# Optimization experiments

Measured on AMD Instinct MI355X. Metric: run time of the kernel, lower is better.

Reference implementation:

```python
import jax, jax.numpy as jnp
import numpy as np

N, D, H_ENC, NZ, K, H_EXP, C = 32768, 1024, 512, 64, 16, 256, 10


def setup_inputs() -> dict:
    key = jax.random.key(0)
    ks = jax.random.split(key, 12)
    s = 0.02
    return {
        "X": jax.random.normal(ks[0], (N, D), dtype=jnp.float32),
        "enc_W": jax.random.normal(ks[1], (D, H_ENC), dtype=jnp.float32) * s,
        "enc_b": jnp.zeros((H_ENC,), dtype=jnp.float32),
        "z_W": jax.random.normal(ks[2], (H_ENC, NZ), dtype=jnp.float32) * s,
        "z_b": jnp.zeros((NZ,), dtype=jnp.float32),
        "mu": jax.random.normal(ks[3], (K, NZ), dtype=jnp.float32),  # cluster_layer
        "W1": jax.random.normal(ks[4], (K, NZ, H_EXP), dtype=jnp.float32) * s,
        "b1": jnp.zeros((K, H_EXP), dtype=jnp.float32),
        "W2": jax.random.normal(ks[5], (K, H_EXP, C), dtype=jnp.float32) * s,
        "b2": jnp.zeros((K, C), dtype=jnp.float32),
    }


def reference(X, enc_W, enc_b, z_W, z_b, mu, W1, b1, W2, b2):
    # AE encoder: Linear-ReLU -> z_layer
    h = jax.nn.relu(X @ enc_W + enc_b)                 # [N, H_ENC]
    z = h @ z_W + z_b                                  # [N, NZ]
    # source_distribution (Student-t, alpha=1; exponent (alpha+1)/2 = 1)
    dist = jnp.sum((z[:, None, :] - mu[None, :, :]) ** 2, axis=-1)  # [N, K]
    q = 1.0 / (1.0 + dist)
    q = q / jnp.sum(q, axis=1, keepdims=True)          # [N, K]
    # per-expert Linear-ReLU-Linear over full batch (attention=True path)
    eh = jax.nn.relu(jnp.einsum("nd,kdh->nkh", z, W1) + b1[None])  # [N, K, H_EXP]
    logits = jnp.einsum("nkh,khc->nkc", eh, W2) + b2[None]         # [N, K, C]
    # soft combine: preds[:, c] += q[:, k] * logits[:, k, c]
    preds = jnp.einsum("nk,nkc->nc", q, logits)        # [N, C]
    return preds
```

## Files before the change

kernel.cpp:

```cpp
#include <hip/hip_runtime.h>
#include <stdint.h>

#define N_ROWS 32768
#define DIM    1024
#define HENC   512
#define NZ     64
#define KE     16
#define HEXP   256
#define NC     10

typedef __attribute__((ext_vector_type(8))) __bf16 bf16x8;
typedef __attribute__((ext_vector_type(4))) float f32x4;
typedef __attribute__((ext_vector_type(8))) unsigned short u16x8;
typedef __attribute__((ext_vector_type(4))) unsigned short u16x4;

__device__ __forceinline__ unsigned short f2bf(float f) {
    __bf16 h = (__bf16)f;
    return __builtin_bit_cast(unsigned short, h);
}

__device__ __forceinline__ void gload_lds16(void* lds, const void* gsrc) {
    __builtin_amdgcn_global_load_lds(
        (const __attribute__((address_space(1))) unsigned int*)gsrc,
        (__attribute__((address_space(3))) unsigned int*)lds,
        16, 0, 0);
}

#define SWZ(col, row) ((col) ^ (((row) & 7) << 3))

__global__ void prep_weights(const float* __restrict__ enc_W,
                             const float* __restrict__ z_W,
                             const float* __restrict__ W1,
                             const float* __restrict__ W2,
                             unsigned short* __restrict__ enc_Wt,
                             unsigned short* __restrict__ z_Wt,
                             unsigned short* __restrict__ W1t,
                             unsigned short* __restrict__ W2t) {
    int i = blockIdx.x * 256 + threadIdx.x;
    if (i < 524288) {
        int n = i >> 10, k = i & 1023;
        enc_Wt[i] = f2bf(enc_W[k * HENC + n]);
    } else if (i < 557056) {
        int i2 = i - 524288;
        int n = i2 >> 9, k = i2 & 511;
        z_Wt[i2] = f2bf(z_W[k * NZ + n]);
    } else if (i < 819200) {
        int i3 = i - 557056;
        int e = i3 >> 14, rem = i3 & 16383;
        int h = rem >> 6, d = rem & 63;
        W1t[i3] = f2bf(W1[(e * NZ + d) * HEXP + h]);
    } else if (i < 884736) {
        int i4 = i - 819200;
        int e = i4 >> 12, rem = i4 & 4095;
        int c = rem >> 8, h = rem & 255;
        W2t[i4] = (c < NC) ? f2bf(W2[(e * HEXP + h) * NC + c]) : (unsigned short)0;
    }
}

__launch_bounds__(256, 2)
__global__ void gemm1(const float* __restrict__ X,
                      const unsigned short* __restrict__ Bt,
                      const float* __restrict__ enc_b,
                      unsigned short* __restrict__ hb) {
    __shared__ unsigned short As[128][64];
    __shared__ unsigned short Bs[2][256][64];
    const int t = threadIdx.x;
    const int lane = t & 63;
    const int w = t >> 6;
    const int g = lane >> 4;
    const int l15 = lane & 15;
    const int l7 = l15 & 7;
    const int wm = (w >> 1) * 64;
    const int wn = (w & 1) * 128;

    const int bid = blockIdx.x;
    const int wgid = (bid & 7) * 64 + (bid >> 3);
    const int m0 = (wgid >> 1) * 128;
    const int n0 = (wgid & 1) * 256;

    const int arow = t >> 4, acolq = t & 15;
    const float* aptr = X + (size_t)(m0 + arow) * DIM + acolq * 4;
    const int ascol = SWZ(acolq * 4, arow);
    const int brow0 = lane >> 3;
    const int bsrccol = SWZ((lane & 7) * 8, brow0);
    const unsigned short* bptr = Bt + (size_t)(n0 + brow0) * DIM + bsrccol;

    f32x4 acc[4][8];
#pragma unroll
    for (int i = 0; i < 4; ++i)
#pragma unroll
        for (int j = 0; j < 8; ++j) acc[i][j] = f32x4{0.f, 0.f, 0.f, 0.f};

    {
#pragma unroll
        for (int it = 0; it < 8; ++it) {
            const int chunk = it * 4 + w;
            gload_lds16(&Bs[0][chunk * 8][0], bptr + (size_t)chunk * 8 * DIM);
        }
        float4 a[8];
#pragma unroll
        for (int it = 0; it < 8; ++it)
            a[it] = *(const float4*)(aptr + (size_t)it * 16 * DIM);
#pragma unroll
        for (int it = 0; it < 8; ++it) {
            u16x4 p;
            p[0] = f2bf(a[it].x); p[1] = f2bf(a[it].y);
            p[2] = f2bf(a[it].z); p[3] = f2bf(a[it].w);
            *(u16x4*)&As[it * 16 + arow][ascol] = p;
        }
    }
    __syncthreads();

    float4 an[8];
    for (int step = 0; step < 16; ++step) {
        const int cur = step & 1, nxt = cur ^ 1;

        if (step < 15) {
            const int k1 = (step + 1) * 64;
#pragma unroll
            for (int it = 0; it < 8; ++it) {
                const int chunk = it * 4 + w;
                gload_lds16(&Bs[nxt][chunk * 8][0],
                            bptr + (size_t)chunk * 8 * DIM + k1);
            }
#pragma unroll
            for (int it = 0; it < 8; ++it)
                an[it] = *(const float4*)(aptr + (size_t)it * 16 * DIM + k1);
        }

#pragma unroll
        for (int kk = 0; kk < 2; ++kk) {
            const int ko = kk * 32 + g * 8;
            const int sko = SWZ(ko, l7);
            bf16x8 af[4], bfr[8];
#pragma unroll
            for (int i = 0; i < 4; ++i)
                af[i] = *(const bf16x8*)&As[wm + i * 16 + l15][sko];
#pragma unroll
            for (int j = 0; j < 8; ++j)
                bfr[j] = *(const bf16x8*)&Bs[cur][wn + j * 16 + l15][sko];
#pragma unroll
            for (int i = 0; i < 4; ++i)
#pragma unroll
                for (int j = 0; j < 8; ++j)
                    acc[i][j] = __builtin_amdgcn_mfma_f32_16x16x32_bf16(af[i], bfr[j], acc[i][j], 0, 0, 0);
        }
        __syncthreads();

        if (step < 15) {
#pragma unroll
            for (int it = 0; it < 8; ++it) {
                u16x4 p;
                p[0] = f2bf(an[it].x); p[1] = f2bf(an[it].y);
                p[2] = f2bf(an[it].z); p[3] = f2bf(an[it].w);
                *(u16x4*)&As[it * 16 + arow][ascol] = p;
            }
        }
        __syncthreads();
    }

#pragma unroll
    for (int j = 0; j < 8; ++j) {
        int col = n0 + wn + j * 16 + l15;
        float bias = enc_b[col];
#pragma unroll
        for (int i = 0; i < 4; ++i) {
            int rbase = m0 + wm + i * 16 + g * 4;
#pragma unroll
            for (int r = 0; r < 4; ++r) {
                float v = acc[i][j][r] + bias;
                v = v > 0.f ? v : 0.f;
                hb[(size_t)(rbase + r) * HENC + col] = f2bf(v);
            }
        }
    }
}

__launch_bounds__(256, 2)
__global__ void gemm2(const unsigned short* __restrict__ hb,
                      const unsigned short* __restrict__ zWt,
                      const float* __restrict__ z_b,
                      float* __restrict__ z) {
    __shared__ unsigned short As2[2][64][64];
    const int t = threadIdx.x, lane = t & 63, w = t >> 6;
    const int g = lane >> 4, l15 = lane & 15;
    const int l7 = l15 & 7;
    const int m0 = blockIdx.x * 64;
    const int brow0 = lane >> 3;
    const int bsrccol = SWZ((lane & 7) * 8, brow0);

    f32x4 acc[4];
#pragma unroll
    for (int j = 0; j < 4; ++j) acc[j] = f32x4{0.f, 0.f, 0.f, 0.f};

#pragma unroll
    for (int it = 0; it < 2; ++it) {
        const int chunk = it * 4 + w;
        gload_lds16(&As2[0][chunk * 8][0],
                    hb + (size_t)(m0 + chunk * 8 + brow0) * HENC + bsrccol);
    }
    __syncthreads();

    for (int step = 0; step < 8; ++step) {
        const int cur = step & 1, nxt = cur ^ 1;
        bf16x8 bfr[2][4];
#pragma unroll
        for (int kk = 0; kk < 2; ++kk) {
            const int kg = step * 64 + kk * 32 + g * 8;
#pragma unroll
            for (int j = 0; j < 4; ++j)
                bfr[kk][j] = *(const bf16x8*)(zWt + (size_t)(j * 16 + l15) * HENC + kg);
        }
        if (step < 7) {
            const int k1 = (step + 1) * 64;
#pragma unroll
            for (int it = 0; it < 2; ++it) {
                const int chunk = it * 4 + w;
                gload_lds16(&As2[nxt][chunk * 8][0],
                            hb + (size_t)(m0 + chunk * 8 + brow0) * HENC + k1 + bsrccol);
            }
        }
#pragma unroll
        for (int kk = 0; kk < 2; ++kk) {
            const int ko = kk * 32 + g * 8;
            bf16x8 af = *(const bf16x8*)&As2[cur][w * 16 + l15][SWZ(ko, l7)];
#pragma unroll
            for (int j = 0; j < 4; ++j)
                acc[j] = __builtin_amdgcn_mfma_f32_16x16x32_bf16(af, bfr[kk][j], acc[j], 0, 0, 0);
        }
        __syncthreads();
    }
#pragma unroll
    for (int j = 0; j < 4; ++j) {
        int col = j * 16 + l15;
        float bias = z_b[col];
#pragma unroll
        for (int r = 0; r < 4; ++r) {
            int row = m0 + w * 16 + g * 4 + r;
            z[(size_t)row * NZ + col] = acc[j][r] + bias;
        }
    }
}

__launch_bounds__(256, 1)
__global__ void expert_kernel(const float* __restrict__ z,
                              const float* __restrict__ mu,
                              const unsigned short* __restrict__ W1t,
                              const float* __restrict__ b1,
                              const unsigned short* __restrict__ W2t,
                              const float* __restrict__ b2,
                              float* __restrict__ out) {
    __shared__ union SU {
        struct { float zs[128][64]; float mus[16][64]; float rn[128]; float mun[16]; } a;
        unsigned short ehs[4][32][264];
    } su;
    __shared__ float qs[128][16];
    __shared__ unsigned short w1s[256][64];
    __shared__ unsigned short w2s[16][256];
    __shared__ float b1s[256];

    const int t = threadIdx.x;
    const int lane = t & 63;
    const int w = t >> 6;
    const int g = lane >> 4;
    const int l15 = lane & 15;
    const int l7 = l15 & 7;
    const int r0 = blockIdx.x * 128;

    {
        const float4* zsrc = (const float4*)(z + (size_t)r0 * NZ);
        float4* zdst = (float4*)&su.a.zs[0][0];
#pragma unroll
        for (int it = 0; it < 8; ++it) zdst[it * 256 + t] = zsrc[it * 256 + t];
        ((float4*)&su.a.mus[0][0])[t] = ((const float4*)mu)[t];
    }
    __syncthreads();
    if (t < 128) {
        float s = 0.f;
        for (int d = 0; d < NZ; ++d) { float v = su.a.zs[t][d]; s += v * v; }
        su.a.rn[t] = s;
    } else if (t < 144) {
        int k = t - 128;
        float s = 0.f;
        for (int d = 0; d < NZ; ++d) { float v = su.a.mus[k][d]; s += v * v; }
        su.a.mun[k] = s;
    }
    __syncthreads();
    bf16x8 az[2][2];
#pragma unroll
    for (int i = 0; i < 2; ++i)
#pragma unroll
        for (int ks = 0; ks < 2; ++ks) {
            int row = w * 32 + i * 16 + l15;
            int ko = ks * 32 + g * 8;
            float4 lo = *(const float4*)&su.a.zs[row][ko];
            float4 hi = *(const float4*)&su.a.zs[row][ko + 4];
            u16x8 tmp;
            tmp[0] = f2bf(lo.x); tmp[1] = f2bf(lo.y); tmp[2] = f2bf(lo.z); tmp[3] = f2bf(lo.w);
            tmp[4] = f2bf(hi.x); tmp[5] = f2bf(hi.y); tmp[6] = f2bf(hi.z); tmp[7] = f2bf(hi.w);
            az[i][ks] = __builtin_bit_cast(bf16x8, tmp);
        }
    {
        bf16x8 bmu[2];
#pragma unroll
        for (int ks = 0; ks < 2; ++ks) {
            int ko = ks * 32 + g * 8;
            float4 lo = *(const float4*)&su.a.mus[l15][ko];
            float4 hi = *(const float4*)&su.a.mus[l15][ko + 4];
            u16x8 tmp;
            tmp[0] = f2bf(lo.x); tmp[1] = f2bf(lo.y); tmp[2] = f2bf(lo.z); tmp[3] = f2bf(lo.w);
            tmp[4] = f2bf(hi.x); tmp[5] = f2bf(hi.y); tmp[6] = f2bf(hi.z); tmp[7] = f2bf(hi.w);
            bmu[ks] = __builtin_bit_cast(bf16x8, tmp);
        }
        f32x4 dacc[2] = {f32x4{0.f, 0.f, 0.f, 0.f}, f32x4{0.f, 0.f, 0.f, 0.f}};
#pragma unroll
        for (int ks = 0; ks < 2; ++ks)
#pragma unroll
            for (int i = 0; i < 2; ++i)
                dacc[i] = __builtin_amdgcn_mfma_f32_16x16x32_bf16(az[i][ks], bmu[ks], dacc[i], 0, 0, 0);
#pragma unroll
        for (int i = 0; i < 2; ++i)
#pragma unroll
            for (int r = 0; r < 4; ++r) {
                int rl = w * 32 + i * 16 + g * 4 + r;
                float dist = su.a.rn[rl] - 2.f * dacc[i][r] + su.a.mun[l15];
                qs[rl][l15] = 1.f / (1.f + dist);
            }
    }
    __syncthreads();
    if (t < 128) {
        float s = 0.f;
#pragma unroll
        for (int k = 0; k < KE; ++k) s += qs[t][k];
        float inv = 1.f / s;
#pragma unroll
        for (int k = 0; k < KE; ++k) qs[t][k] *= inv;
    }
    __syncthreads();
    float pacc[2][4];
#pragma unroll
    for (int i = 0; i < 2; ++i)
#pragma unroll
        for (int r = 0; r < 4; ++r) pacc[i][r] = 0.f;

    for (int e = 0; e < KE; ++e) {
        {
            const uint4* s1 = (const uint4*)(W1t + e * (NZ * HEXP));
#pragma unroll
            for (int it = 0; it < 8; ++it) {
                int f = it * 256 + t;
                int row = f >> 3;
                *(uint4*)&w1s[row][SWZ((f & 7) * 8, row)] = s1[f];
            }
            const uint4* s2 = (const uint4*)(W2t + e * (16 * HEXP));
#pragma unroll
            for (int it = 0; it < 2; ++it) {
                int f = it * 256 + t;
                int row = f >> 5;
                *(uint4*)&w2s[row][SWZ((f & 31) * 8, row)] = s2[f];
            }
            b1s[t] = b1[e * HEXP + t];
        }
        __syncthreads();
        f32x4 ea[2][16];
#pragma unroll
        for (int i = 0; i < 2; ++i)
#pragma unroll
            for (int j = 0; j < 16; ++j) ea[i][j] = f32x4{0.f, 0.f, 0.f, 0.f};
#pragma unroll
        for (int ks = 0; ks < 2; ++ks) {
            const int ko = ks * 32 + g * 8;
            const int sko = SWZ(ko, l7);
#pragma unroll
            for (int j = 0; j < 16; ++j) {
                bf16x8 bw = *(const bf16x8*)&w1s[j * 16 + l15][sko];
#pragma unroll
                for (int i = 0; i < 2; ++i)
                    ea[i][j] = __builtin_amdgcn_mfma_f32_16x16x32_bf16(az[i][ks], bw, ea[i][j], 0, 0, 0);
            }
        }
#pragma unroll
        for (int j = 0; j < 16; ++j) {
            int h = j * 16 + l15;
            float bias = b1s[h];
#pragma unroll
            for (int i = 0; i < 2; ++i)
#pragma unroll
                for (int r = 0; r < 4; ++r) {
                    float v = ea[i][j][r] + bias;
                    v = v > 0.f ? v : 0.f;
                    su.ehs[w][i * 16 + g * 4 + r][h] = f2bf(v);
                }
        }
        __syncthreads();
        f32x4 la[2] = {f32x4{0.f, 0.f, 0.f, 0.f}, f32x4{0.f, 0.f, 0.f, 0.f}};
#pragma unroll
        for (int ks = 0; ks < 8; ++ks) {
            const int ko = ks * 32 + g * 8;
            bf16x8 bw2 = *(const bf16x8*)&w2s[l15][SWZ(ko, l7)];
#pragma unroll
            for (int i = 0; i < 2; ++i) {
                bf16x8 ae = *(const bf16x8*)&su.ehs[w][i * 16 + l15][ko];
                la[i] = __builtin_amdgcn_mfma_f32_16x16x32_bf16(ae, bw2, la[i], 0, 0, 0);
            }
        }
        float b2v = (l15 < NC) ? b2[e * NC + l15] : 0.f;
#pragma unroll
        for (int i = 0; i < 2; ++i)
#pragma unroll
            for (int r = 0; r < 4; ++r) {
                int rl = w * 32 + i * 16 + g * 4 + r;
                pacc[i][r] += qs[rl][e] * (la[i][r] + b2v);
            }
        __syncthreads();
    }
    if (l15 < NC) {
#pragma unroll
        for (int i = 0; i < 2; ++i)
#pragma unroll
            for (int r = 0; r < 4; ++r) {
                int row = r0 + w * 32 + i * 16 + g * 4 + r;
                out[(size_t)row * NC + l15] = pacc[i][r];
            }
    }
}

extern "C" void kernel_launch(void* const* d_in, const int* in_sizes, int n_in,
                              void* d_out, int out_size, void* d_ws, size_t ws_size,
                              hipStream_t stream) {
    const float* X     = (const float*)d_in[0];
    const float* enc_W = (const float*)d_in[1];
    const float* enc_b = (const float*)d_in[2];
    const float* z_W   = (const float*)d_in[3];
    const float* z_b   = (const float*)d_in[4];
    const float* mu    = (const float*)d_in[5];
    const float* W1    = (const float*)d_in[6];
    const float* b1    = (const float*)d_in[7];
    const float* W2    = (const float*)d_in[8];
    const float* b2    = (const float*)d_in[9];
    float* out = (float*)d_out;

    char* ws = (char*)d_ws;
    unsigned short* hb     = (unsigned short*)(ws);
    float*          z      = (float*)(ws + 33554432);
    unsigned short* enc_Wt = (unsigned short*)(ws + 41943040);
    unsigned short* z_Wt   = (unsigned short*)(ws + 42991616);
    unsigned short* W1t    = (unsigned short*)(ws + 43057152);
    unsigned short* W2t    = (unsigned short*)(ws + 43581440);

    prep_weights<<<dim3(3456), dim3(256), 0, stream>>>(enc_W, z_W, W1, W2,
                                                       enc_Wt, z_Wt, W1t, W2t);
    gemm1<<<dim3(512), dim3(256), 0, stream>>>(X, enc_Wt, enc_b, hb);
    gemm2<<<dim3(512), dim3(256), 0, stream>>>(hb, z_Wt, z_b, z);
    expert_kernel<<<dim3(256), dim3(256), 0, stream>>>(z, mu, W1t, b1, W2t, b2, out);
}
```

Measured before the change: 149.8 us.

## Restructure expert kernel: 64-row blocks, direct global weight loads, no per-expert LDS staging

The expert kernel now processes 64 rows per block with 512 blocks instead of 128 rows with 256 blocks, so more blocks can fill the GPU's compute units. It also drops the shared-memory staging of W1/W2/b1 and the per-expert block barriers. Each wave instead reads the bf16 weights directly from global memory (served mostly from cache) and computes the hidden layer in two halves of 128 to cut register pressure, which allows two blocks per CU. The cost is redundant global and cache weight traffic across waves, uncoalesced 16-byte weight loads, and smaller MFMA reuse per weight fragment.

After: 216.3 us. +44.4%, slower.

```diff
diff --git a/kernel.cpp b/kernel.cpp
--- a/kernel.cpp
+++ b/kernel.cpp
@@ -242,7 +242,7 @@
     }
 }
 
-__launch_bounds__(256, 1)
+__launch_bounds__(256, 2)
 __global__ void expert_kernel(const float* __restrict__ z,
                               const float* __restrict__ mu,
                               const unsigned short* __restrict__ W1t,
@@ -250,56 +250,68 @@
                               const unsigned short* __restrict__ W2t,
                               const float* __restrict__ b2,
                               float* __restrict__ out) {
-    __shared__ union SU {
-        struct { float zs[128][64]; float mus[16][64]; float rn[128]; float mun[16]; } a;
-        unsigned short ehs[4][32][264];
+    __shared__ __align__(16) union SU {
+        struct {
+            float zs[64][68];
+            float mus[16][68];
+            float rn[64];
+            float mun[16];
+        } a;
+        unsigned short ehs[4][16][136];
     } su;
-    __shared__ float qs[128][16];
-    __shared__ unsigned short w1s[256][64];
-    __shared__ unsigned short w2s[16][256];
-    __shared__ float b1s[256];
+    __shared__ float qs[64][16];
 
     const int t = threadIdx.x;
     const int lane = t & 63;
     const int w = t >> 6;
     const int g = lane >> 4;
     const int l15 = lane & 15;
-    const int l7 = l15 & 7;
-    const int r0 = blockIdx.x * 128;
+    const int r0 = blockIdx.x * 64;
 
     {
-        const float4* zsrc = (const float4*)(z + (size_t)r0 * NZ);
-        float4* zdst = (float4*)&su.a.zs[0][0];
-#pragma unroll
-        for (int it = 0; it < 8; ++it) zdst[it * 256 + t] = zsrc[it * 256 + t];
-        ((float4*)&su.a.mus[0][0])[t] = ((const float4*)mu)[t];
-    }
-    __syncthreads();
-    if (t < 128) {
+#pragma unroll
+        for (int it = 0; it < 4; ++it) {
+            int idx = it * 256 + t;
+            int r = idx >> 4, c = (idx & 15) * 4;
+            *(float4*)&su.a.zs[r][c] = *(const float4*)(z + (size_t)(r0 + r) * NZ + c);
+        }
+        int r = t >> 4, c = (t & 15) * 4;
+        *(float4*)&su.a.mus[r][c] = *(const float4*)(mu + (size_t)r * NZ + c);
+    }
+    __syncthreads();
+
+    if (t < 64) {
         float s = 0.f;
-        for (int d = 0; d < NZ; ++d) { float v = su.a.zs[t][d]; s += v * v; }
+#pragma unroll
+        for (int dq = 0; dq < 16; ++dq) {
+            float4 v = *(const float4*)&su.a.zs[t][dq * 4];
+            s += v.x * v.x + v.y * v.y + v.z * v.z + v.w * v.w;
+        }
         su.a.rn[t] = s;
-    } else if (t < 144) {
-        int k = t - 128;
+    } else if (t < 80) {
+        int k = t - 64;
         float s = 0.f;
-        for (int d = 0; d < NZ; ++d) { float v = su.a.mus[k][d]; s += v * v; }
+#pragma unroll
+        for (int dq = 0; dq < 16; ++dq) {
+            float4 v = *(const float4*)&su.a.mus[k][dq * 4];
+            s += v.x * v.x + v.y * v.y + v.z * v.z + v.w * v.w;
+        }
         su.a.mun[k] = s;
     }
     __syncthreads();
-    bf16x8 az[2][2];
-#pragma unroll
-    for (int i = 0; i < 2; ++i)
-#pragma unroll
-        for (int ks = 0; ks < 2; ++ks) {
-            int row = w * 32 + i * 16 + l15;
-            int ko = ks * 32 + g * 8;
-            float4 lo = *(const float4*)&su.a.zs[row][ko];
-            float4 hi = *(const float4*)&su.a.zs[row][ko + 4];
-            u16x8 tmp;
-            tmp[0] = f2bf(lo.x); tmp[1] = f2bf(lo.y); tmp[2] = f2bf(lo.z); tmp[3] = f2bf(lo.w);
-            tmp[4] = f2bf(hi.x); tmp[5] = f2bf(hi.y); tmp[6] = f2bf(hi.z); tmp[7] = f2bf(hi.w);
-            az[i][ks] = __builtin_bit_cast(bf16x8, tmp);
-        }
+
+    bf16x8 az[2];
+#pragma unroll
+    for (int ks = 0; ks < 2; ++ks) {
+        int row = w * 16 + l15;
+        int ko = ks * 32 + g * 8;
+        float4 lo = *(const float4*)&su.a.zs[row][ko];
+        float4 hi = *(const float4*)&su.a.zs[row][ko + 4];
+        u16x8 tmp;
+        tmp[0] = f2bf(lo.x); tmp[1] = f2bf(lo.y); tmp[2] = f2bf(lo.z); tmp[3] = f2bf(lo.w);
+        tmp[4] = f2bf(hi.x); tmp[5] = f2bf(hi.y); tmp[6] = f2bf(hi.z); tmp[7] = f2bf(hi.w);
+        az[ks] = __builtin_bit_cast(bf16x8, tmp);
+    }
     {
         bf16x8 bmu[2];
 #pragma unroll
@@ -312,23 +324,20 @@
             tmp[4] = f2bf(hi.x); tmp[5] = f2bf(hi.y); tmp[6] = f2bf(hi.z); tmp[7] = f2bf(hi.w);
             bmu[ks] = __builtin_bit_cast(bf16x8, tmp);
         }
-        f32x4 dacc[2] = {f32x4{0.f, 0.f, 0.f, 0.f}, f32x4{0.f, 0.f, 0.f, 0.f}};
+        f32x4 dacc = f32x4{0.f, 0.f, 0.f, 0.f};
 #pragma unroll
         for (int ks = 0; ks < 2; ++ks)
-#pragma unroll
-            for (int i = 0; i < 2; ++i)
-                dacc[i] = __builtin_amdgcn_mfma_f32_16x16x32_bf16(az[i][ks], bmu[ks], dacc[i], 0, 0, 0);
-#pragma unroll
-        for (int i = 0; i < 2; ++i)
-#pragma unroll
-            for (int r = 0; r < 4; ++r) {
-                int rl = w * 32 + i * 16 + g * 4 + r;
-                float dist = su.a.rn[rl] - 2.f * dacc[i][r] + su.a.mun[l15];
-                qs[rl][l15] = 1.f / (1.f + dist);
-            }
-    }
-    __syncthreads();
-    if (t < 128) {
+            dacc = __builtin_amdgcn_mfma_f32_16x16x32_bf16(az[ks], bmu[ks], dacc, 0, 0, 0);
+#pragma unroll
+        for (int r = 0; r < 4; ++r) {
+            int rl = w * 16 + g * 4 + r;
+            float dist = su.a.rn[rl] - 2.f * dacc[r] + su.a.mun[l15];
+            qs[rl][l15] = 1.f / (1.f + dist);
+        }
+    }
+    __syncthreads();
+
+    if (t < 64) {
         float s = 0.f;
 #pragma unroll
         for (int k = 0; k < KE; ++k) s += qs[t][k];
@@ -337,91 +346,60 @@
         for (int k = 0; k < KE; ++k) qs[t][k] *= inv;
     }
     __syncthreads();
-    float pacc[2][4];
-#pragma unroll
-    for (int i = 0; i < 2; ++i)
-#pragma unroll
-        for (int r = 0; r < 4; ++r) pacc[i][r] = 0.f;
+
+    float pacc[4] = {0.f, 0.f, 0.f, 0.f};
+    unsigned short* eh = &su.ehs[w][0][0];
 
     for (int e = 0; e < KE; ++e) {
-        {
-            const uint4* s1 = (const uint4*)(W1t + e * (NZ * HEXP));
-#pragma unroll
-            for (int it = 0; it < 8; ++it) {
-                int f = it * 256 + t;
-                int row = f >> 3;
-                *(uint4*)&w1s[row][SWZ((f & 7) * 8, row)] = s1[f];
-            }
-            const uint4* s2 = (const uint4*)(W2t + e * (16 * HEXP));
-#pragma unroll
-            for (int it = 0; it < 2; ++it) {
-                int f = it * 256 + t;
-                int row = f >> 5;
-                *(uint4*)&w2s[row][SWZ((f & 31) * 8, row)] = s2[f];
-            }
-            b1s[t] = b1[e * HEXP + t];
-        }
-        __syncthreads();
-        f32x4 ea[2][16];
-#pragma unroll
-        for (int i = 0; i < 2; ++i)
-#pragma unroll
-            for (int j = 0; j < 16; ++j) ea[i][j] = f32x4{0.f, 0.f, 0.f, 0.f};
-#pragma unroll
-        for (int ks = 0; ks < 2; ++ks) {
-            const int ko = ks * 32 + g * 8;
-            const int sko = SWZ(ko, l7);
-#pragma unroll
-            for (int j = 0; j < 16; ++j) {
-                bf16x8 bw = *(const bf16x8*)&w1s[j * 16 + l15][sko];
-#pragma unroll
-                for (int i = 0; i < 2; ++i)
-                    ea[i][j] = __builtin_amdgcn_mfma_f32_16x16x32_bf16(az[i][ks], bw, ea[i][j], 0, 0, 0);
-            }
-        }
-#pragma unroll
-        for (int j = 0; j < 16; ++j) {
-            int h = j * 16 + l15;
-            float bias = b1s[h];
-#pragma unroll
-            for (int i = 0; i < 2; ++i)
+        const unsigned short* w1e = W1t + e * (HEXP * NZ);
+        const unsigned short* w2e = W2t + e * (16 * HEXP);
+        f32x4 la = f32x4{0.f, 0.f, 0.f, 0.f};
+
+#pragma unroll
+        for (int half = 0; half < 2; ++half) {
+            const int h0 = half * 128;
+            f32x4 ea[8];
+#pragma unroll
+            for (int j = 0; j < 8; ++j) ea[j] = f32x4{0.f, 0.f, 0.f, 0.f};
+#pragma unroll
+            for (int j = 0; j < 8; ++j) {
+                const unsigned short* wp = w1e + (size_t)(h0 + j * 16 + l15) * NZ + g * 8;
+                bf16x8 w1a = *(const bf16x8*)wp;
+                bf16x8 w1b = *(const bf16x8*)(wp + 32);
+                ea[j] = __builtin_amdgcn_mfma_f32_16x16x32_bf16(az[0], w1a, ea[j], 0, 0, 0);
+                ea[j] = __builtin_amdgcn_mfma_f32_16x16x32_bf16(az[1], w1b, ea[j], 0, 0, 0);
+            }
+#pragma unroll
+            for (int j = 0; j < 8; ++j) {
+                float bias = b1[e * HEXP + h0 + j * 16 + l15];
 #pragma unroll
                 for (int r = 0; r < 4; ++r) {
-                    float v = ea[i][j][r] + bias;
+                    float v = ea[j][r] + bias;
                     v = v > 0.f ? v : 0.f;
-                    su.ehs[w][i * 16 + g * 4 + r][h] = f2bf(v);
+                    eh[(g * 4 + r) * 136 + j * 16 + l15] = f2bf(v);
                 }
-        }
-        __syncthreads();
-        f32x4 la[2] = {f32x4{0.f, 0.f, 0.f, 0.f}, f32x4{0.f, 0.f, 0.f, 0.f}};
-#pragma unroll
-        for (int ks = 0; ks < 8; ++ks) {
-            const int ko = ks * 32 + g * 8;
-            bf16x8 bw2 = *(const bf16x8*)&w2s[l15][SWZ(ko, l7)];
-#pragma unroll
-            for (int i = 0; i < 2; ++i) {
-                bf16x8 ae = *(const bf16x8*)&su.ehs[w][i * 16 + l15][ko];
-                la[i] = __builtin_amdgcn_mfma_f32_16x16x32_bf16(ae, bw2, la[i], 0, 0, 0);
+            }
+#pragma unroll
+            for (int ks2 = 0; ks2 < 4; ++ks2) {
+                bf16x8 ef = *(const bf16x8*)&eh[l15 * 136 + ks2 * 32 + g * 8];
+                bf16x8 w2f = *(const bf16x8*)(w2e + (size_t)l15 * HEXP + h0 + ks2 * 32 + g * 8);
+                la = __builtin_amdgcn_mfma_f32_16x16x32_bf16(ef, w2f, la, 0, 0, 0);
             }
         }
         float b2v = (l15 < NC) ? b2[e * NC + l15] : 0.f;
 #pragma unroll
-        for (int i = 0; i < 2; ++i)
-#pragma unroll
-            for (int r = 0; r < 4; ++r) {
-                int rl = w * 32 + i * 16 + g * 4 + r;
-                pacc[i][r] += qs[rl][e] * (la[i][r] + b2v);
-            }
-        __syncthreads();
-    }
+        for (int r = 0; r < 4; ++r) {
+            int rl = w * 16 + g * 4 + r;
+            pacc[r] += qs[rl][e] * (la[r] + b2v);
+        }
+    }
+
     if (l15 < NC) {
 #pragma unroll
-        for (int i = 0; i < 2; ++i)
-#pragma unroll
-            for (int r = 0; r < 4; ++r) {
-                int row = r0 + w * 32 + i * 16 + g * 4 + r;
-                out[(size_t)row * NC + l15] = pacc[i][r];
-            }
+        for (int r = 0; r < 4; ++r) {
+            int row = r0 + w * 16 + g * 4 + r;
+            out[(size_t)row * NC + l15] = pacc[r];
+        }
     }
 }
 
@@ -452,5 +430,5 @@
                                                        enc_Wt, z_Wt, W1t, W2t);
     gemm1<<<dim3(512), dim3(256), 0, stream>>>(X, enc_Wt, enc_b, hb);
     gemm2<<<dim3(512), dim3(256), 0, stream>>>(hb, z_Wt, z_b, z);
-    expert_kernel<<<dim3(256), dim3(256), 0, stream>>>(z, mu, W1t, b1, W2t, b2, out);
-}
+    expert_kernel<<<dim3(512), dim3(256), 0, stream>>>(z, mu, W1t, b1, W2t, b2, out);
+}
```
